# Kernel tuning notes

Measured on AMD Instinct MI355X. Metric: run time of the kernel, lower is better.

Reference implementation:

```python
import jax, jax.numpy as jnp
import numpy as np

FEAT_STRIDE = 16
NMS_THRESH = 0.7
PRE_NMS = 6000   # eval mode: n_test_pre_nms
POST_NMS = 300   # eval mode: n_test_post_nms
MIN_SIZE = 16
NEG = jnp.float32(-1e30)


def _base_anchors(base_size=16, ratios=(0.5, 1.0, 2.0), scales=(8, 16, 32)):
    ctr = (base_size - 1) / 2.0
    size = float(base_size * base_size)
    out = []
    for r in ratios:
        w = np.round(np.sqrt(size / r))
        h = np.round(w * r)
        for s in scales:
            ws, hs = w * s, h * s
            out.append([ctr - 0.5 * (ws - 1), ctr - 0.5 * (hs - 1),
                        ctr + 0.5 * (ws - 1), ctr + 0.5 * (hs - 1)])
    return np.asarray(out, dtype=np.float32)  # (9,4)


def _all_anchors(feat_h, feat_w):
    base = _base_anchors()
    sx = np.arange(feat_w, dtype=np.float32) * FEAT_STRIDE
    sy = np.arange(feat_h, dtype=np.float32) * FEAT_STRIDE
    gx, gy = np.meshgrid(sx, sy)                      # (H,W)
    shifts = np.stack([gx, gy, gx, gy], axis=-1).reshape(-1, 1, 4)
    anchors = (shifts + base[None, :, :]).reshape(-1, 4)  # (H*W*9,4), order (h,w,a)
    return jnp.asarray(anchors)


def _nms_keep(boxes):
    # boxes sorted by descending score; torchvision IoU convention (no +1)
    n = boxes.shape[0]
    area = (boxes[:, 2] - boxes[:, 0]) * (boxes[:, 3] - boxes[:, 1])
    lt = jnp.maximum(boxes[:, None, :2], boxes[None, :, :2])  # (N,N,2)
    rb = jnp.minimum(boxes[:, None, 2:], boxes[None, :, 2:])
    wh = jnp.clip(rb - lt, 0.0)
    inter = wh[..., 0] * wh[..., 1]
    iou = inter / (area[:, None] + area[None, :] - inter)
    over = iou > NMS_THRESH
    idx = jnp.arange(n)

    def body(i, supp):
        row = over[i] & (idx > i) & jnp.logical_not(supp[i])
        return supp | row

    supp = jax.lax.fori_loop(0, n, body, jnp.zeros((n,), bool))
    keep = jnp.nonzero(~supp, size=POST_NMS, fill_value=0)[0]
    return keep


def reference(rpn_cls_scores, rpn_bbox_preds, img_h, img_w):
    feat_h, feat_w = rpn_cls_scores.shape[2], rpn_cls_scores.shape[3]
    anchors = _all_anchors(feat_h, feat_w)                      # (K,4)
    scores = jax.nn.softmax(
        rpn_cls_scores.transpose(0, 2, 3, 1).reshape(-1, 2), axis=1)[:, 1]
    deltas = rpn_bbox_preds.transpose(0, 2, 3, 1).reshape(-1, 4)

    widths = anchors[:, 2] - anchors[:, 0] + 1.0
    heights = anchors[:, 3] - anchors[:, 1] + 1.0
    ctr_x = anchors[:, 0] + 0.5 * widths
    ctr_y = anchors[:, 1] + 0.5 * heights
    dx, dy, dw, dh = deltas[:, 0], deltas[:, 1], deltas[:, 2], deltas[:, 3]
    pcx = dx * widths + ctr_x
    pcy = dy * heights + ctr_y
    pw = jnp.exp(dw) * widths
    ph = jnp.exp(dh) * heights

    x1 = jnp.clip(pcx - 0.5 * pw, 0.0, img_w - 1)
    y1 = jnp.clip(pcy - 0.5 * ph, 0.0, img_h - 1)
    x2 = jnp.clip(pcx + 0.5 * pw, 0.0, img_w - 1)
    y2 = jnp.clip(pcy + 0.5 * ph, 0.0, img_h - 1)
    proposals = jnp.stack([x1, y1, x2, y2], axis=1)             # (K,4)

    valid = ((x2 - x1 + 1.0) >= MIN_SIZE) & ((y2 - y1 + 1.0) >= MIN_SIZE)
    masked = jnp.where(valid, scores, NEG)
    _, order = jax.lax.top_k(masked, PRE_NMS)                   # sort desc + pre-nms cut
    boxes = proposals[order]                                    # (PRE_NMS,4)

    keep = _nms_keep(boxes)
    kept = boxes[keep]                                          # (POST_NMS,4)
    batch_inds = jnp.zeros((POST_NMS, 1), dtype=kept.dtype)
    return jnp.concatenate([batch_inds, kept], axis=1)          # (POST_NMS,5)


def setup_inputs() -> dict:
    key = jax.random.key(0)
    k1, k2 = jax.random.split(key)
    rpn_cls_scores = jax.random.normal(k1, (1, 18, 64, 100), dtype=jnp.float32)
    rpn_bbox_preds = 0.2 * jax.random.normal(k2, (1, 36, 64, 100), dtype=jnp.float32)
    return {"rpn_cls_scores": rpn_cls_scores, "rpn_bbox_preds": rpn_bbox_preds,
            "img_h": 1024, "img_w": 1600}
```

## Files before the change

### kernel.cpp

```cpp
#include <hip/hip_runtime.h>

typedef unsigned long long u64;
typedef unsigned int u32;

#define FEAT_W 100
#define NANCH 9
#define NTOT 57600
#define NPAD 65536
#define PRE_NMS 6000
#define POST_NMS 300
#define NBLK 94
#define NCHUNK 24
#define CH_STRIDE 6400
#define CHUNK 1024
#define CAP 6144

__constant__ double c_base[9][4] = {
    {-84.0, -40.0, 99.0, 55.0},    {-176.0, -88.0, 191.0, 103.0},
    {-360.0, -184.0, 375.0, 199.0},{-56.0, -56.0, 71.0, 71.0},
    {-120.0, -120.0, 135.0, 135.0},{-248.0, -248.0, 263.0, 263.0},
    {-36.0, -80.0, 51.0, 95.0},    {-80.0, -168.0, 95.0, 183.0},
    {-168.0, -344.0, 183.0, 359.0}};

struct BoxD { double x1, y1, x2, y2; };

__device__ __forceinline__ int packed_off(int i) {
  int q = i >> 6, r = i & 63;
  return 94 * i - 32 * q * (q - 1) - r * q;
}

__device__ __forceinline__ BoxD decode_box(int i, const float* __restrict__ bbox,
                                           double imw1, double imh1) {
  int pos = i / NANCH;
  int a = i - pos * NANCH;
  int h = pos / FEAT_W;
  int w = pos - h * FEAT_W;
  double ax1 = c_base[a][0] + 16.0 * (double)w;
  double ay1 = c_base[a][1] + 16.0 * (double)h;
  double ax2 = c_base[a][2] + 16.0 * (double)w;
  double ay2 = c_base[a][3] + 16.0 * (double)h;
  double wd = ax2 - ax1 + 1.0;
  double hg = ay2 - ay1 + 1.0;
  double cx = ax1 + 0.5 * wd;
  double cy = ay1 + 0.5 * hg;
  const float* bp = bbox + (size_t)(4 * a) * CH_STRIDE + pos;
  double dx = (double)bp[0];
  double dy = (double)bp[CH_STRIDE];
  double dw = (double)bp[2 * CH_STRIDE];
  double dh = (double)bp[3 * CH_STRIDE];
  double pcx = dx * wd + cx;
  double pcy = dy * hg + cy;
  double pw = exp(dw) * wd;
  double ph = exp(dh) * hg;
  BoxD b;
  b.x1 = fmin(fmax(pcx - 0.5 * pw, 0.0), imw1);
  b.y1 = fmin(fmax(pcy - 0.5 * ph, 0.0), imh1);
  b.x2 = fmin(fmax(pcx + 0.5 * pw, 0.0), imw1);
  b.y2 = fmin(fmax(pcy + 0.5 * ph, 0.0), imh1);
  return b;
}

__device__ __forceinline__ u64 score_key(int i, const float* __restrict__ cls,
                                         const float* __restrict__ bbox,
                                         double imw1, double imh1) {
  BoxD b = decode_box(i, bbox, imw1, imh1);
  bool valid = (b.x2 - b.x1 + 1.0 >= 16.0) && (b.y2 - b.y1 + 1.0 >= 16.0);
  int pos = i / NANCH;
  int a = i - pos * NANCH;
  double c0 = (double)cls[(size_t)(2 * a) * CH_STRIDE + pos];
  double c1 = (double)cls[(size_t)(2 * a + 1) * CH_STRIDE + pos];
  double m = fmax(c0, c1);
  double e0 = exp(c0 - m), e1 = exp(c1 - m);
  double s = e1 / (e0 + e1);
  double masked = valid ? s : (double)(-1e30f);
  u64 u = (u64)__double_as_longlong(masked);
  return (u >> 63) ? ~u : (u | 0x8000000000000000ULL);
}

__device__ __forceinline__ bool before(u64 ka, u32 va, u64 kb, u32 vb) {
  return (ka > kb) || (ka == kb && va < vb);
}
__device__ __forceinline__ bool comes_after(u64 ka, u32 va, u64 kb, u32 vb) {
  return (ka < kb) || (ka == kb && va > vb);
}

__global__ __launch_bounds__(512) void k_score_sort(
    const float* __restrict__ cls, const float* __restrict__ bbox,
    const int* __restrict__ imh, const int* __restrict__ imw,
    u64* __restrict__ keys, u32* __restrict__ vals) {
  __shared__ u64 sk[CHUNK];
  __shared__ u32 sv[CHUNK];
  int base = blockIdx.x * CHUNK;
  double imh1 = (double)(imh[0] - 1);
  double imw1 = (double)(imw[0] - 1);
  for (int t = threadIdx.x; t < CHUNK; t += 512) {
    int i = base + t;
    if (i < NTOT) { sk[t] = score_key(i, cls, bbox, imw1, imh1); sv[t] = (u32)i; }
    else { sk[t] = 0ULL; sv[t] = (u32)i; }
  }
  __syncthreads();
  bool prev_cross = false;
  for (int k = 2; k <= CHUNK; k <<= 1) {
    for (int j = k >> 1; j > 0; j >>= 1) {
      bool cross = (j >= 128);
      if (cross || prev_cross) __syncthreads();
      int t = threadIdx.x;
      int i = ((t & ~(j - 1)) << 1) | (t & (j - 1));
      int l = i | j;
      bool up = ((i & k) == 0);
      u64 ka = sk[i], kb = sk[l];
      u32 va = sv[i], vb = sv[l];
      if (comes_after(ka, va, kb, vb) == up) { sk[i] = kb; sv[i] = vb; sk[l] = ka; sv[l] = va; }
      prev_cross = cross;
    }
  }
  __syncthreads();
  for (int t = threadIdx.x; t < CHUNK; t += 512) { keys[base + t] = sk[t]; vals[base + t] = sv[t]; }
}

__global__ void k_merge1(const u64* __restrict__ Ak, const u32* __restrict__ Av,
                         u64* __restrict__ Bk, u32* __restrict__ Bv) {
  int gtid = blockIdx.x * blockDim.x + threadIdx.x;
  if (gtid >= NPAD) return;
  int lst = gtid >> 10, pos = gtid & 1023, grp = lst >> 2;
  u64 k = Ak[gtid]; u32 v = Av[gtid];
  int b0 = grp << 2;
  int q = lst & 3;
  int i0 = 0 + (0 >= q), i1 = 1 + (1 >= q), i2 = 2 + (2 >= q);
  const u64* K0 = Ak + (size_t)(b0 + i0) * 1024;
  const u64* K1 = Ak + (size_t)(b0 + i1) * 1024;
  const u64* K2 = Ak + (size_t)(b0 + i2) * 1024;
  const u32* V0 = Av + (size_t)(b0 + i0) * 1024;
  const u32* V1 = Av + (size_t)(b0 + i1) * 1024;
  const u32* V2 = Av + (size_t)(b0 + i2) * 1024;
  int lo0 = 0, hi0 = 1024, lo1 = 0, hi1 = 1024, lo2 = 0, hi2 = 1024;
  #pragma unroll
  for (int st = 0; st < 11; ++st) {
    int m0 = (lo0 + hi0) >> 1, m1 = (lo1 + hi1) >> 1, m2 = (lo2 + hi2) >> 1;
    int c0 = min(m0, 1023), c1 = min(m1, 1023), c2 = min(m2, 1023);
    u64 k0 = K0[c0], k1 = K1[c1], k2 = K2[c2];
    u32 v0 = V0[c0], v1 = V1[c1], v2 = V2[c2];
    if (lo0 < hi0) { if (before(k0, v0, k, v)) lo0 = m0 + 1; else hi0 = m0; }
    if (lo1 < hi1) { if (before(k1, v1, k, v)) lo1 = m1 + 1; else hi1 = m1; }
    if (lo2 < hi2) { if (before(k2, v2, k, v)) lo2 = m2 + 1; else hi2 = m2; }
  }
  int rank = pos + lo0 + lo1 + lo2;
  Bk[(size_t)grp * 4096 + rank] = k;
  Bv[(size_t)grp * 4096 + rank] = v;
}

__global__ void k_merge2(const u64* __restrict__ Bk, const u32* __restrict__ Bv,
                         u64* __restrict__ Ak, u32* __restrict__ Av) {
  int gtid = blockIdx.x * blockDim.x + threadIdx.x;
  if (gtid >= NPAD) return;
  int lst = gtid >> 12, pos = gtid & 4095, grp = lst >> 2;
  u64 k = Bk[gtid]; u32 v = Bv[gtid];
  int b0 = grp << 2;
  int q = lst & 3;
  int i0 = 0 + (0 >= q), i1 = 1 + (1 >= q), i2 = 2 + (2 >= q);
  const u64* K0 = Bk + (size_t)(b0 + i0) * 4096;
  const u64* K1 = Bk + (size_t)(b0 + i1) * 4096;
  const u64* K2 = Bk + (size_t)(b0 + i2) * 4096;
  const u32* V0 = Bv + (size_t)(b0 + i0) * 4096;
  const u32* V1 = Bv + (size_t)(b0 + i1) * 4096;
  const u32* V2 = Bv + (size_t)(b0 + i2) * 4096;
  int lo0 = 0, hi0 = 4096, lo1 = 0, hi1 = 4096, lo2 = 0, hi2 = 4096;
  #pragma unroll
  for (int st = 0; st < 13; ++st) {
    int m0 = (lo0 + hi0) >> 1, m1 = (lo1 + hi1) >> 1, m2 = (lo2 + hi2) >> 1;
    int c0 = min(m0, 4095), c1 = min(m1, 4095), c2 = min(m2, 4095);
    u64 k0 = K0[c0], k1 = K1[c1], k2 = K2[c2];
    u32 v0 = V0[c0], v1 = V1[c1], v2 = V2[c2];
    if (lo0 < hi0) { if (before(k0, v0, k, v)) lo0 = m0 + 1; else hi0 = m0; }
    if (lo1 < hi1) { if (before(k1, v1, k, v)) lo1 = m1 + 1; else hi1 = m1; }
    if (lo2 < hi2) { if (before(k2, v2, k, v)) lo2 = m2 + 1; else hi2 = m2; }
  }
  int rank = pos + lo0 + lo1 + lo2;
  if (rank < CAP) { Ak[(size_t)grp * CAP + rank] = k; Av[(size_t)grp * CAP + rank] = v; }
}

__global__ void k_merge3(const u64* __restrict__ Ak, const u32* __restrict__ Av,
                         const float* __restrict__ bbox, const int* __restrict__ imh,
                         const int* __restrict__ imw, float4* __restrict__ fboxes) {
  int gtid = blockIdx.x * blockDim.x + threadIdx.x;
  if (gtid >= 4 * CAP) return;
  int lst = gtid / CAP, pos = gtid - lst * CAP;
  u64 k = Ak[gtid]; u32 v = Av[gtid];
  int i0 = 0 + (0 >= lst), i1 = 1 + (1 >= lst), i2 = 2 + (2 >= lst);
  const u64* K0 = Ak + (size_t)i0 * CAP;
  const u64* K1 = Ak + (size_t)i1 * CAP;
  const u64* K2 = Ak + (size_t)i2 * CAP;
  const u32* V0 = Av + (size_t)i0 * CAP;
  const u32* V1 = Av + (size_t)i1 * CAP;
  const u32* V2 = Av + (size_t)i2 * CAP;
  int lo0 = 0, hi0 = CAP, lo1 = 0, hi1 = CAP, lo2 = 0, hi2 = CAP;
  #pragma unroll
  for (int st = 0; st < 13; ++st) {
    int m0 = (lo0 + hi0) >> 1, m1 = (lo1 + hi1) >> 1, m2 = (lo2 + hi2) >> 1;
    int c0 = min(m0, CAP - 1), c1 = min(m1, CAP - 1), c2 = min(m2, CAP - 1);
    u64 k0 = K0[c0], k1 = K1[c1], k2 = K2[c2];
    u32 v0 = V0[c0], v1 = V1[c1], v2 = V2[c2];
    if (lo0 < hi0) { if (before(k0, v0, k, v)) lo0 = m0 + 1; else hi0 = m0; }
    if (lo1 < hi1) { if (before(k1, v1, k, v)) lo1 = m1 + 1; else hi1 = m1; }
    if (lo2 < hi2) { if (before(k2, v2, k, v)) lo2 = m2 + 1; else hi2 = m2; }
  }
  int rank = pos + lo0 + lo1 + lo2;
  if (rank < PRE_NMS) {
    double imh1 = (double)(imh[0] - 1);
    double imw1 = (double)(imw[0] - 1);
    BoxD b = decode_box((int)v, bbox, imw1, imh1);
    fboxes[rank] = make_float4((float)b.x1, (float)b.y1, (float)b.x2, (float)b.y2);
  }
}

__global__ void k_mask(const float4* __restrict__ fboxes, u64* __restrict__ mask,
                       u64* __restrict__ colC) {
  __shared__ float4 cb[64];
  int bc = blockIdx.x, br = blockIdx.y;
  int t = threadIdx.x;
  bool samechunk = (bc >> 2) == (br >> 2);
  if (bc < br) {
    if (samechunk) colC[(size_t)(((bc << 6) + t) * 4 + (br & 3))] = 0;
    return;
  }
  int j0 = bc * 64;
  int jt = j0 + t;
  cb[t] = (jt < PRE_NMS) ? fboxes[jt] : make_float4(0.f, 0.f, 0.f, 0.f);
  __syncthreads();
  int i = br * 64 + t;
  u64 bits = 0;
  if (i < PRE_NMS) {
    float4 rb = fboxes[i];
    float areai = (rb.z - rb.x) * (rb.w - rb.y);
    int cmax = min(64, PRE_NMS - j0);
    for (int c = 0; c < cmax; ++c) {
      int j = j0 + c;
      if (j <= i) continue;
      float4 cbx = cb[c];
      float xx1 = fmaxf(rb.x, cbx.x), yy1 = fmaxf(rb.y, cbx.y);
      float xx2 = fminf(rb.z, cbx.z), yy2 = fminf(rb.w, cbx.w);
      float w = fmaxf(xx2 - xx1, 0.0f), h = fmaxf(yy2 - yy1, 0.0f);
      float inter = w * h;
      float areaj = (cbx.z - cbx.x) * (cbx.w - cbx.y);
      float iou = inter / (areai + areaj - inter);
      if (iou > 0.7f) bits |= (1ULL << c);
    }
    mask[(size_t)(packed_off(i) + (bc - br))] = bits;
  }
  if (samechunk) {
    u64 colbits = 0;
    for (int j2 = 0; j2 < 64; ++j2) {
      u64 bl = __ballot(((bits >> j2) & 1ULL) != 0);
      if (t == j2) colbits = bl;
    }
    colC[(size_t)(((bc << 6) + t) * 4 + (br & 3))] = colbits;
  }
}

__device__ __forceinline__ u64 valid_word(int w) {
  int base = w << 6;
  if (base >= PRE_NMS) return 0ULL;
  if (base + 64 <= PRE_NMS) return ~0ULL;
  return (1ULL << (PRE_NMS - base)) - 1ULL;
}

__global__ __launch_bounds__(64) void k_scan(const u64* __restrict__ mask,
                                             const u64* __restrict__ colC,
                                             const float4* __restrict__ fboxes,
                                             float* __restrict__ out) {
  __shared__ int keepIdx[384];
  __shared__ int keepA[384];
  int lane = threadIdx.x;
  for (int r = lane; r < 384; r += 64) { keepIdx[r] = 0; keepA[r] = 0; }
  int nkeep = 0;
  bool done = false;
  int a0 = 0, a1 = 0, a2 = 0, a3 = 0, a4 = 0;
  u64 or0 = 0, or1 = 0, or2 = 0, or3 = 0;

  u64 ct00, ct01, ct02, ct03, ct10, ct11, ct12, ct13;
  u64 ct20, ct21, ct22, ct23, ct30, ct31, ct32, ct33;

#define COL_LOAD(cc, T, x0, x1, x2, x3)                                        \
  {                                                                            \
    int J_ = ((cc) << 8) + ((T) << 6) + lane;                                  \
    x0 = 0; x1 = 0; x2 = 0; x3 = 0;                                            \
    if (J_ < PRE_NMS) {                                                        \
      const ulonglong2* p_ = (const ulonglong2*)(colC + (size_t)J_ * 4);       \
      ulonglong2 u_ = p_[0], w_ = p_[1];                                       \
      x0 = u_.x; x1 = u_.y; x2 = w_.x; x3 = w_.y;                              \
    }                                                                          \
  }

  COL_LOAD(0, 0, ct00, ct01, ct02, ct03)
  COL_LOAD(0, 1, ct10, ct11, ct12, ct13)
  COL_LOAD(0, 2, ct20, ct21, ct22, ct23)
  COL_LOAD(0, 3, ct30, ct31, ct32, ct33)

  for (int c = 0; c < NCHUNK && !done; ++c) {
    int wbase = c << 2;
    int wnext = wbase + 4;
    bool gnext = (c + 1 < NCHUNK);
    bool tail_n = (wnext + 2) < NBLK;
    int oldn = nkeep;

    u64 n00 = 0, n01 = 0, n02 = 0, n03 = 0, n10 = 0, n11 = 0, n12 = 0, n13 = 0;
    u64 n20 = 0, n21 = 0, n22 = 0, n23 = 0, n30 = 0, n31 = 0, n32 = 0, n33 = 0;
    if (gnext) {
      COL_LOAD(c + 1, 0, n00, n01, n02, n03)
      COL_LOAD(c + 1, 1, n10, n11, n12, n13)
      COL_LOAD(c + 1, 2, n20, n21, n22, n23)
      COL_LOAD(c + 1, 3, n30, n31, n32, n33)
    }

    u64 e0 = 0, e1 = 0, e2 = 0, e3 = 0;
    if (gnext) {
#define EGATHER(AA, LIM)                                                       \
      if ((LIM) < oldn) {                                                      \
        const u64* p_ = mask + (size_t)(AA) + wnext;                           \
        e0 |= p_[0]; e1 |= p_[1];                                              \
        if (tail_n) { e2 |= p_[2]; e3 |= p_[3]; }                              \
      }
      EGATHER(a0, lane)
      EGATHER(a1, 64 + lane)
      EGATHER(a2, 128 + lane)
      EGATHER(a3, 192 + lane)
      EGATHER(a4, 256 + lane)
#undef EGATHER
    }

    u64 kf0 = 0, kf1 = 0, kf2 = 0, kf3 = 0;

#define RUN_WORD(OR_, TT, DIAGC, CROSS_EXPR, KFVAR)                            \
    if (!done) {                                                               \
      u64 alive = ~(OR_) & valid_word(wbase + (TT));                           \
      alive &= ~__ballot((CROSS_EXPR) != 0ULL);                                \
      u64 kfacc = 0;                                                           \
      while (alive) {                                                          \
        int b = __builtin_ctzll(alive);                                        \
        u64 bb = 1ULL << b;                                                    \
        kfacc |= bb;                                                           \
        u64 sup_ = __ballot((((DIAGC) >> b) & 1ULL) != 0ULL);                  \
        alive &= ~(sup_ | bb);                                                 \
      }                                                                        \
      KFVAR = kfacc;                                                           \
      if (kfacc) {                                                             \
        if ((kfacc >> lane) & 1ULL) {                                          \
          int idx = nkeep + __popcll(kfacc & ((1ULL << lane) - 1ULL));         \
          if (idx < 384) {                                                     \
            int K = (c << 8) + ((TT) << 6) + lane;                             \
            keepIdx[idx] = K;                                                  \
            keepA[idx] = packed_off(K) - (K >> 6);                             \
          }                                                                    \
        }                                                                      \
        nkeep += __popcll(kfacc);                                              \
        if (nkeep >= POST_NMS) done = true;                                    \
      }                                                                        \
    }

    RUN_WORD(or0, 0, ct00, 0ULL, kf0)
    RUN_WORD(or1, 1, ct11, (ct10 & kf0), kf1)
    RUN_WORD(or2, 2, ct22, (ct20 & kf0) | (ct21 & kf1), kf2)
    RUN_WORD(or3, 3, ct33, (ct30 & kf0) | (ct31 & kf1) | (ct32 & kf2), kf3)
#undef RUN_WORD
    (void)kf3;

    if (gnext && !done) {
      int nk = min(nkeep, 384);
#define LGATHER(AR, SLOT)                                                      \
      {                                                                        \
        int s_ = (SLOT);                                                       \
        if (s_ >= oldn && s_ < nk) {                                           \
          AR = keepA[s_];                                                      \
          const u64* p_ = mask + (size_t)AR + wnext;                           \
          e0 |= p_[0]; e1 |= p_[1];                                            \
          if (tail_n) { e2 |= p_[2]; e3 |= p_[3]; }                            \
        }                                                                      \
      }
      LGATHER(a0, lane)
      LGATHER(a1, 64 + lane)
      LGATHER(a2, 128 + lane)
      LGATHER(a3, 192 + lane)
      LGATHER(a4, 256 + lane)
#undef LGATHER
      #pragma unroll
      for (int m = 32; m; m >>= 1) {
        e0 |= __shfl_xor(e0, m);
        e1 |= __shfl_xor(e1, m);
        e2 |= __shfl_xor(e2, m);
        e3 |= __shfl_xor(e3, m);
      }
      or0 = e0; or1 = e1; or2 = e2; or3 = e3;
    }

    ct00 = n00; ct01 = n01; ct02 = n02; ct03 = n03;
    ct10 = n10; ct11 = n11; ct12 = n12; ct13 = n13;
    ct20 = n20; ct21 = n21; ct22 = n22; ct23 = n23;
    ct30 = n30; ct31 = n31; ct32 = n32; ct33 = n33;
  }
#undef COL_LOAD
  __syncthreads();

  for (int r = lane; r < POST_NMS; r += 64) {
    int kk = keepIdx[r];
    float4 b = fboxes[kk];
    float* o = out + r * 5;
    o[0] = 0.0f;
    o[1] = b.x;
    o[2] = b.y;
    o[3] = b.z;
    o[4] = b.w;
  }
}

extern "C" void kernel_launch(void* const* d_in, const int* in_sizes, int n_in,
                              void* d_out, int out_size, void* d_ws, size_t ws_size,
                              hipStream_t stream) {
  const float* cls = (const float*)d_in[0];
  const float* bbox = (const float*)d_in[1];
  const int* imh = (const int*)d_in[2];
  const int* imw = (const int*)d_in[3];
  float* out = (float*)d_out;

  char* p = (char*)d_ws;
  float4* fboxes = (float4*)p;
  u64* colC = (u64*)(p + 96256);
  char* mb = p + 385024;
  u64* maskbuf = (u64*)mb;
  u64* Ak = (u64*)mb;
  u32* Av = (u32*)(mb + 524288);
  u64* Bk = (u64*)(mb + 786432);
  u32* Bv = (u32*)(mb + 1310720);

  k_score_sort<<<64, 512, 0, stream>>>(cls, bbox, imh, imw, Ak, Av);
  k_merge1<<<NPAD / 256, 256, 0, stream>>>(Ak, Av, Bk, Bv);
  k_merge2<<<NPAD / 256, 256, 0, stream>>>(Bk, Bv, Ak, Av);
  k_merge3<<<(4 * CAP) / 256, 256, 0, stream>>>(Ak, Av, bbox, imh, imw, fboxes);
  k_mask<<<dim3(NBLK, NBLK), 64, 0, stream>>>(fboxes, maskbuf, colC);
  k_scan<<<1, 64, 0, stream>>>(maskbuf, colC, fboxes, out);
}
```

Before: 148.5 us.

## Merge sorted runs 8-way in two passes and rank by logit difference

The merge stage now uses two 8-way merge passes (1024→8192 runs, then a final 8-way merge that decodes the top boxes) instead of three 4-way passes. This drops one kernel launch and one global read-write round trip, at the cost of seven binary searches per element instead of three. The sort key is also replaced by the logit difference c1-c0, which orders the same as the softmax probability, so the exp and divide per anchor go away. Ties that come from float rounding of the softmax may now break differently.

```diff
diff --git a/kernel.cpp b/kernel.cpp
--- a/kernel.cpp
+++ b/kernel.cpp
@@ -13,7 +13,6 @@
 #define NCHUNK 24
 #define CH_STRIDE 6400
 #define CHUNK 1024
-#define CAP 6144
 
 __constant__ double c_base[9][4] = {
     {-84.0, -40.0, 99.0, 55.0},    {-176.0, -88.0, 191.0, 103.0},
@@ -69,10 +68,7 @@
   int a = i - pos * NANCH;
   double c0 = (double)cls[(size_t)(2 * a) * CH_STRIDE + pos];
   double c1 = (double)cls[(size_t)(2 * a + 1) * CH_STRIDE + pos];
-  double m = fmax(c0, c1);
-  double e0 = exp(c0 - m), e1 = exp(c1 - m);
-  double s = e1 / (e0 + e1);
-  double masked = valid ? s : (double)(-1e30f);
+  double masked = valid ? (c1 - c0) : -1e30;
   u64 u = (u64)__double_as_longlong(masked);
   return (u >> 63) ? ~u : (u | 0x8000000000000000ULL);
 }
@@ -118,93 +114,82 @@
   for (int t = threadIdx.x; t < CHUNK; t += 512) { keys[base + t] = sk[t]; vals[base + t] = sv[t]; }
 }
 
+template <int N, int STEPS>
+__device__ __forceinline__ int rank7(
+    const u64* __restrict__ K0, const u32* __restrict__ V0,
+    const u64* __restrict__ K1, const u32* __restrict__ V1,
+    const u64* __restrict__ K2, const u32* __restrict__ V2,
+    const u64* __restrict__ K3, const u32* __restrict__ V3,
+    const u64* __restrict__ K4, const u32* __restrict__ V4,
+    const u64* __restrict__ K5, const u32* __restrict__ V5,
+    const u64* __restrict__ K6, const u32* __restrict__ V6,
+    u64 k, u32 v) {
+  int lo0 = 0, hi0 = N, lo1 = 0, hi1 = N, lo2 = 0, hi2 = N;
+  int lo3 = 0, hi3 = N, lo4 = 0, hi4 = N, lo5 = 0, hi5 = N;
+  int lo6 = 0, hi6 = N;
+  #pragma unroll
+  for (int st = 0; st < STEPS; ++st) {
+    int m0 = (lo0 + hi0) >> 1, m1 = (lo1 + hi1) >> 1, m2 = (lo2 + hi2) >> 1;
+    int m3 = (lo3 + hi3) >> 1, m4 = (lo4 + hi4) >> 1, m5 = (lo5 + hi5) >> 1;
+    int m6 = (lo6 + hi6) >> 1;
+    int c0 = min(m0, N - 1), c1 = min(m1, N - 1), c2 = min(m2, N - 1);
+    int c3 = min(m3, N - 1), c4 = min(m4, N - 1), c5 = min(m5, N - 1);
+    int c6 = min(m6, N - 1);
+    u64 k0 = K0[c0], k1 = K1[c1], k2 = K2[c2], k3 = K3[c3];
+    u64 k4 = K4[c4], k5 = K5[c5], k6 = K6[c6];
+    u32 v0 = V0[c0], v1 = V1[c1], v2 = V2[c2], v3 = V3[c3];
+    u32 v4 = V4[c4], v5 = V5[c5], v6 = V6[c6];
+    if (lo0 < hi0) { if (before(k0, v0, k, v)) lo0 = m0 + 1; else hi0 = m0; }
+    if (lo1 < hi1) { if (before(k1, v1, k, v)) lo1 = m1 + 1; else hi1 = m1; }
+    if (lo2 < hi2) { if (before(k2, v2, k, v)) lo2 = m2 + 1; else hi2 = m2; }
+    if (lo3 < hi3) { if (before(k3, v3, k, v)) lo3 = m3 + 1; else hi3 = m3; }
+    if (lo4 < hi4) { if (before(k4, v4, k, v)) lo4 = m4 + 1; else hi4 = m4; }
+    if (lo5 < hi5) { if (before(k5, v5, k, v)) lo5 = m5 + 1; else hi5 = m5; }
+    if (lo6 < hi6) { if (before(k6, v6, k, v)) lo6 = m6 + 1; else hi6 = m6; }
+  }
+  return lo0 + lo1 + lo2 + lo3 + lo4 + lo5 + lo6;
+}
+
 __global__ void k_merge1(const u64* __restrict__ Ak, const u32* __restrict__ Av,
                          u64* __restrict__ Bk, u32* __restrict__ Bv) {
   int gtid = blockIdx.x * blockDim.x + threadIdx.x;
   if (gtid >= NPAD) return;
-  int lst = gtid >> 10, pos = gtid & 1023, grp = lst >> 2;
+  int lst = gtid >> 10, pos = gtid & 1023, grp = lst >> 3;
   u64 k = Ak[gtid]; u32 v = Av[gtid];
-  int b0 = grp << 2;
-  int q = lst & 3;
+  int b0 = grp << 3, q = lst & 7;
   int i0 = 0 + (0 >= q), i1 = 1 + (1 >= q), i2 = 2 + (2 >= q);
-  const u64* K0 = Ak + (size_t)(b0 + i0) * 1024;
-  const u64* K1 = Ak + (size_t)(b0 + i1) * 1024;
-  const u64* K2 = Ak + (size_t)(b0 + i2) * 1024;
-  const u32* V0 = Av + (size_t)(b0 + i0) * 1024;
-  const u32* V1 = Av + (size_t)(b0 + i1) * 1024;
-  const u32* V2 = Av + (size_t)(b0 + i2) * 1024;
-  int lo0 = 0, hi0 = 1024, lo1 = 0, hi1 = 1024, lo2 = 0, hi2 = 1024;
-  #pragma unroll
-  for (int st = 0; st < 11; ++st) {
-    int m0 = (lo0 + hi0) >> 1, m1 = (lo1 + hi1) >> 1, m2 = (lo2 + hi2) >> 1;
-    int c0 = min(m0, 1023), c1 = min(m1, 1023), c2 = min(m2, 1023);
-    u64 k0 = K0[c0], k1 = K1[c1], k2 = K2[c2];
-    u32 v0 = V0[c0], v1 = V1[c1], v2 = V2[c2];
-    if (lo0 < hi0) { if (before(k0, v0, k, v)) lo0 = m0 + 1; else hi0 = m0; }
-    if (lo1 < hi1) { if (before(k1, v1, k, v)) lo1 = m1 + 1; else hi1 = m1; }
-    if (lo2 < hi2) { if (before(k2, v2, k, v)) lo2 = m2 + 1; else hi2 = m2; }
-  }
-  int rank = pos + lo0 + lo1 + lo2;
-  Bk[(size_t)grp * 4096 + rank] = k;
-  Bv[(size_t)grp * 4096 + rank] = v;
+  int i3 = 3 + (3 >= q), i4 = 4 + (4 >= q), i5 = 5 + (5 >= q);
+  int i6 = 6 + (6 >= q);
+  int rank = pos + rank7<1024, 11>(
+      Ak + (size_t)(b0 + i0) * 1024, Av + (size_t)(b0 + i0) * 1024,
+      Ak + (size_t)(b0 + i1) * 1024, Av + (size_t)(b0 + i1) * 1024,
+      Ak + (size_t)(b0 + i2) * 1024, Av + (size_t)(b0 + i2) * 1024,
+      Ak + (size_t)(b0 + i3) * 1024, Av + (size_t)(b0 + i3) * 1024,
+      Ak + (size_t)(b0 + i4) * 1024, Av + (size_t)(b0 + i4) * 1024,
+      Ak + (size_t)(b0 + i5) * 1024, Av + (size_t)(b0 + i5) * 1024,
+      Ak + (size_t)(b0 + i6) * 1024, Av + (size_t)(b0 + i6) * 1024, k, v);
+  Bk[(size_t)grp * 8192 + rank] = k;
+  Bv[(size_t)grp * 8192 + rank] = v;
 }
 
 __global__ void k_merge2(const u64* __restrict__ Bk, const u32* __restrict__ Bv,
-                         u64* __restrict__ Ak, u32* __restrict__ Av) {
-  int gtid = blockIdx.x * blockDim.x + threadIdx.x;
-  if (gtid >= NPAD) return;
-  int lst = gtid >> 12, pos = gtid & 4095, grp = lst >> 2;
-  u64 k = Bk[gtid]; u32 v = Bv[gtid];
-  int b0 = grp << 2;
-  int q = lst & 3;
-  int i0 = 0 + (0 >= q), i1 = 1 + (1 >= q), i2 = 2 + (2 >= q);
-  const u64* K0 = Bk + (size_t)(b0 + i0) * 4096;
-  const u64* K1 = Bk + (size_t)(b0 + i1) * 4096;
-  const u64* K2 = Bk + (size_t)(b0 + i2) * 4096;
-  const u32* V0 = Bv + (size_t)(b0 + i0) * 4096;
-  const u32* V1 = Bv + (size_t)(b0 + i1) * 4096;
-  const u32* V2 = Bv + (size_t)(b0 + i2) * 4096;
-  int lo0 = 0, hi0 = 4096, lo1 = 0, hi1 = 4096, lo2 = 0, hi2 = 4096;
-  #pragma unroll
-  for (int st = 0; st < 13; ++st) {
-    int m0 = (lo0 + hi0) >> 1, m1 = (lo1 + hi1) >> 1, m2 = (lo2 + hi2) >> 1;
-    int c0 = min(m0, 4095), c1 = min(m1, 4095), c2 = min(m2, 4095);
-    u64 k0 = K0[c0], k1 = K1[c1], k2 = K2[c2];
-    u32 v0 = V0[c0], v1 = V1[c1], v2 = V2[c2];
-    if (lo0 < hi0) { if (before(k0, v0, k, v)) lo0 = m0 + 1; else hi0 = m0; }
-    if (lo1 < hi1) { if (before(k1, v1, k, v)) lo1 = m1 + 1; else hi1 = m1; }
-    if (lo2 < hi2) { if (before(k2, v2, k, v)) lo2 = m2 + 1; else hi2 = m2; }
-  }
-  int rank = pos + lo0 + lo1 + lo2;
-  if (rank < CAP) { Ak[(size_t)grp * CAP + rank] = k; Av[(size_t)grp * CAP + rank] = v; }
-}
-
-__global__ void k_merge3(const u64* __restrict__ Ak, const u32* __restrict__ Av,
                          const float* __restrict__ bbox, const int* __restrict__ imh,
                          const int* __restrict__ imw, float4* __restrict__ fboxes) {
   int gtid = blockIdx.x * blockDim.x + threadIdx.x;
-  if (gtid >= 4 * CAP) return;
-  int lst = gtid / CAP, pos = gtid - lst * CAP;
-  u64 k = Ak[gtid]; u32 v = Av[gtid];
+  if (gtid >= NPAD) return;
+  int lst = gtid >> 13, pos = gtid & 8191;
+  u64 k = Bk[gtid]; u32 v = Bv[gtid];
   int i0 = 0 + (0 >= lst), i1 = 1 + (1 >= lst), i2 = 2 + (2 >= lst);
-  const u64* K0 = Ak + (size_t)i0 * CAP;
-  const u64* K1 = Ak + (size_t)i1 * CAP;
-  const u64* K2 = Ak + (size_t)i2 * CAP;
-  const u32* V0 = Av + (size_t)i0 * CAP;
-  const u32* V1 = Av + (size_t)i1 * CAP;
-  const u32* V2 = Av + (size_t)i2 * CAP;
-  int lo0 = 0, hi0 = CAP, lo1 = 0, hi1 = CAP, lo2 = 0, hi2 = CAP;
-  #pragma unroll
-  for (int st = 0; st < 13; ++st) {
-    int m0 = (lo0 + hi0) >> 1, m1 = (lo1 + hi1) >> 1, m2 = (lo2 + hi2) >> 1;
-    int c0 = min(m0, CAP - 1), c1 = min(m1, CAP - 1), c2 = min(m2, CAP - 1);
-    u64 k0 = K0[c0], k1 = K1[c1], k2 = K2[c2];
-    u32 v0 = V0[c0], v1 = V1[c1], v2 = V2[c2];
-    if (lo0 < hi0) { if (before(k0, v0, k, v)) lo0 = m0 + 1; else hi0 = m0; }
-    if (lo1 < hi1) { if (before(k1, v1, k, v)) lo1 = m1 + 1; else hi1 = m1; }
-    if (lo2 < hi2) { if (before(k2, v2, k, v)) lo2 = m2 + 1; else hi2 = m2; }
-  }
-  int rank = pos + lo0 + lo1 + lo2;
+  int i3 = 3 + (3 >= lst), i4 = 4 + (4 >= lst), i5 = 5 + (5 >= lst);
+  int i6 = 6 + (6 >= lst);
+  int rank = pos + rank7<8192, 14>(
+      Bk + (size_t)i0 * 8192, Bv + (size_t)i0 * 8192,
+      Bk + (size_t)i1 * 8192, Bv + (size_t)i1 * 8192,
+      Bk + (size_t)i2 * 8192, Bv + (size_t)i2 * 8192,
+      Bk + (size_t)i3 * 8192, Bv + (size_t)i3 * 8192,
+      Bk + (size_t)i4 * 8192, Bv + (size_t)i4 * 8192,
+      Bk + (size_t)i5 * 8192, Bv + (size_t)i5 * 8192,
+      Bk + (size_t)i6 * 8192, Bv + (size_t)i6 * 8192, k, v);
   if (rank < PRE_NMS) {
     double imh1 = (double)(imh[0] - 1);
     double imw1 = (double)(imw[0] - 1);
@@ -433,8 +418,7 @@
 
   k_score_sort<<<64, 512, 0, stream>>>(cls, bbox, imh, imw, Ak, Av);
   k_merge1<<<NPAD / 256, 256, 0, stream>>>(Ak, Av, Bk, Bv);
-  k_merge2<<<NPAD / 256, 256, 0, stream>>>(Bk, Bv, Ak, Av);
-  k_merge3<<<(4 * CAP) / 256, 256, 0, stream>>>(Ak, Av, bbox, imh, imw, fboxes);
+  k_merge2<<<NPAD / 256, 256, 0, stream>>>(Bk, Bv, bbox, imh, imw, fboxes);
   k_mask<<<dim3(NBLK, NBLK), 64, 0, stream>>>(fboxes, maskbuf, colC);
   k_scan<<<1, 64, 0, stream>>>(maskbuf, colC, fboxes, out);
 }
```

Result: slower. 151.6 us (+2.1%).
